# Optimization experiments

Hardware: AMD Instinct MI355X
Metric: run time of the kernel (lower is better)

Reference implementation:

```python
import jax, jax.numpy as jnp
import numpy as np
from jax import lax

B, S, D = 4, 2048, 512          # batch, doc seq len, input_size
Y = 8922                          # num labels (ICD codes)
V, E = 50000, 100                 # vocab, word embed dim
T, K = 32, 9                      # code-title tokens, conv filter size
PAD = K // 2


def setup_inputs() -> dict:
    key = jax.random.key(0)
    ks = jax.random.split(key, 8)
    x = jax.random.normal(ks[0], (B, S, D), dtype=jnp.float32)
    target = jax.random.randint(ks[1], (B, Y), 0, 2).astype(jnp.float32)
    c2title = jax.random.randint(ks[2], (Y, T), 0, V)
    embed_W = jax.random.normal(ks[3], (V, E), dtype=jnp.float32) * 0.1
    conv_w = jax.random.normal(ks[4], (D, E, K), dtype=jnp.float32) * 0.05  # [out, in, k]
    conv_b = jax.random.normal(ks[5], (D,), dtype=jnp.float32) * 0.05
    final_w = jax.random.normal(ks[6], (Y, D), dtype=jnp.float32) * 0.05
    final_b = jax.random.normal(ks[7], (Y,), dtype=jnp.float32) * 0.05
    return {"x": x, "target": target, "c2title": c2title, "embed_W": embed_W,
            "conv_w": conv_w, "conv_b": conv_b, "final_w": final_w, "final_b": final_b}


def reference(x, target, c2title, embed_W, conv_w, conv_b, final_w, final_b):
    # Code-title encoder: embed -> Conv1d (same padding) -> max-pool over time -> tanh
    ct = embed_W[c2title]                      # [Y, T, E]
    ct = jnp.transpose(ct, (0, 2, 1))          # [Y, E, T]  (NCH)
    U = lax.conv_general_dilated(ct, conv_w, window_strides=(1,),
                                 padding=[(PAD, PAD)],
                                 dimension_numbers=("NCH", "OIH", "NCH"))
    U = U + conv_b[None, :, None]              # [Y, D, T]
    U = jnp.tanh(jnp.max(U, axis=-1))          # [Y, D]  (MaxPool1d(T) + tanh)

    # Label cross-attention over document tokens
    scale = 1.0 / jnp.sqrt(jnp.float32(D))
    scores = jnp.einsum("yd,bsd->bys", U, x) * scale   # [B, Y, S]
    alpha = jax.nn.softmax(scores, axis=-1)             # softmax over seq
    m = jnp.einsum("bys,bsd->byd", alpha, x)            # [B, Y, D]

    # Per-label elementwise dot product + bias
    y = jnp.einsum("byd,yd->by", m, final_w) + final_b  # [B, Y]

    # BCEWithLogitsLoss (mean), numerically stable
    loss = jnp.mean(jnp.maximum(y, 0.0) - y * target + jnp.log1p(jnp.exp(-jnp.abs(y))))
    return (y, loss, alpha, m)
```

## Files before the change

kernel.cpp:

```cpp
#include <hip/hip_runtime.h>
#include <math.h>

#define BQ 4
#define SQ 2048
#define DQ 512
#define YQ 8922
#define TQ 32
#define EQ 100
#define EP 128
#define KQ 9
#define LD 128
#define TP 40
#define YPAD 8960

typedef float f32x4 __attribute__((ext_vector_type(4)));
typedef short s16x8 __attribute__((ext_vector_type(8)));

static __device__ __forceinline__ f32x4 mfma16(s16x8 a, s16x8 b, f32x4 c) {
  return __builtin_amdgcn_mfma_f32_16x16x32_bf16(a, b, c, 0, 0, 0);
}

static __device__ __forceinline__ ushort f2bf(float f) {
  union { float f; unsigned u; } v; v.f = f;
  unsigned r = (v.u + 0x7FFFu + ((v.u >> 16) & 1u)) >> 16;
  return (ushort)r;
}

static __device__ __forceinline__ float bf2f(ushort h) {
  union { unsigned u; float f; } v; v.u = ((unsigned)h) << 16; return v.f;
}

static __device__ __forceinline__ f32x4 ld4u(const float* p) {
  f32x4 v; __builtin_memcpy(&v, p, 16); return v;
}

static __device__ __forceinline__ int swz_chunk(int row, int chunk) {
  return chunk ^ (row & 15);
}
static __device__ __forceinline__ int swz3(int row, int chunk) {
  return chunk ^ (row & 7);
}

__global__ void k_prep_x(const float* __restrict__ x, ushort* __restrict__ xb,
                         ushort* __restrict__ xT) {
  __shared__ ushort sm[32][33];
  int b = blockIdx.z;
  int s0 = blockIdx.x * 32;
  int d0 = blockIdx.y * 32;
  int tx = threadIdx.x, ty = threadIdx.y;
  float v = x[((size_t)b * SQ + s0 + ty) * DQ + d0 + tx];
  ushort h = f2bf(v);
  xb[((size_t)b * SQ + s0 + ty) * DQ + d0 + tx] = h;
  sm[ty][tx] = h;
  __syncthreads();
  xT[((size_t)b * DQ + d0 + ty) * SQ + s0 + tx] = sm[tx][ty];
}

__global__ void k_pack_w(const float* __restrict__ cw, ushort* __restrict__ Wp) {
  int i = blockIdx.x * 256 + threadIdx.x;
  if (i >= KQ * DQ * EP) return;
  int e = i & (EP - 1);
  int d = (i >> 7) & (DQ - 1);
  int kk = i >> 16;
  float v = (e < EQ) ? cw[((size_t)d * EQ + e) * KQ + kk] : 0.f;
  Wp[i] = f2bf(v);
}

__launch_bounds__(256, 2)
__global__ void k_conv(const int* __restrict__ c2t, const float* __restrict__ embed,
                       const ushort* __restrict__ Wp, const float* __restrict__ cb,
                       ushort* __restrict__ U) {
  __shared__ ushort sA[4 * TP * LD];
  __shared__ ushort sB[128 * LD];
  const f32x4 fz4 = {0.f, 0.f, 0.f, 0.f};
  int tid = threadIdx.x;
  int d0 = blockIdx.x * 128;
  int y0 = blockIdx.y * 4;
  int lane = tid & 63, wave = tid >> 6;
  int wm = wave & 1, wn = wave >> 1;
  int lr = lane & 15, lg = lane >> 4;

  #pragma unroll
  for (int it = 0; it < 2; ++it) {
    int u = tid + it * 256;
    if (u < 2 * 4 * TP) {
      int row = u >> 1, half = u & 1;
      int yl = row / TP, tt = row - yl * TP;
      int ts = tt - 4;
      int y = y0 + yl;
      const float* src = 0;
      if (y < YQ && (unsigned)ts < (unsigned)TQ)
        src = embed + (size_t)c2t[y * TQ + ts] * EQ + half * 64;
      #pragma unroll
      for (int j = 0; j < 16; ++j) {
        int col = half * 64 + j * 4;
        f32x4 v = fz4;
        if (src != 0 && col + 4 <= EQ) v = *(const f32x4*)(src + j * 4);
        ushort4 h = make_ushort4(f2bf(v.x), f2bf(v.y), f2bf(v.z), f2bf(v.w));
        int pc = swz_chunk(row, col >> 3);
        *(ushort4*)&sA[row * LD + pc * 8 + (col & 7)] = h;
      }
    }
  }

  s16x8 breg[8];
  {
    const ushort* src = Wp + (size_t)d0 * EP;
    #pragma unroll
    for (int it = 0; it < 8; ++it) {
      int gi = tid + it * 256, r = gi >> 4, g = gi & 15;
      breg[it] = *(const s16x8*)(src + (size_t)r * EP + g * 8);
    }
    #pragma unroll
    for (int it = 0; it < 8; ++it) {
      int gi = tid + it * 256, r = gi >> 4, g = gi & 15;
      *(s16x8*)&sB[r * LD + swz_chunk(r, g) * 8] = breg[it];
    }
  }
  __syncthreads();

  f32x4 acc[4][4];
  #pragma unroll
  for (int i = 0; i < 4; ++i)
    #pragma unroll
    for (int j = 0; j < 4; ++j) acc[i][j] = fz4;

  for (int kk = 0; kk < KQ; ++kk) {
    if (kk + 1 < KQ) {
      const ushort* src = Wp + ((size_t)(kk + 1) * DQ + d0) * EP;
      #pragma unroll
      for (int it = 0; it < 8; ++it) {
        int gi = tid + it * 256, r = gi >> 4, g = gi & 15;
        breg[it] = *(const s16x8*)(src + (size_t)r * EP + g * 8);
      }
    }
    #pragma unroll
    for (int ee = 0; ee < 4; ++ee) {
      s16x8 af[4], bfr[4];
      #pragma unroll
      for (int i = 0; i < 4; ++i) {
        int rowm = wm * 64 + i * 16 + lr;
        int yl = rowm >> 5;
        int row = yl * TP + (rowm & 31) + kk;
        af[i] = *(const s16x8*)&sA[row * LD + swz_chunk(row, ee * 4 + lg) * 8];
      }
      #pragma unroll
      for (int i = 0; i < 4; ++i) {
        int row = wn * 64 + i * 16 + lr;
        bfr[i] = *(const s16x8*)&sB[row * LD + swz_chunk(row, ee * 4 + lg) * 8];
      }
      #pragma unroll
      for (int i = 0; i < 4; ++i)
        #pragma unroll
        for (int j = 0; j < 4; ++j)
          acc[i][j] = mfma16(af[i], bfr[j], acc[i][j]);
    }
    __syncthreads();
    if (kk + 1 < KQ) {
      #pragma unroll
      for (int it = 0; it < 8; ++it) {
        int gi = tid + it * 256, r = gi >> 4, g = gi & 15;
        *(s16x8*)&sB[r * LD + swz_chunk(r, g) * 8] = breg[it];
      }
      __syncthreads();
    }
  }

  const float scl = 0.04419417382415922f;
  #pragma unroll
  for (int L2 = 0; L2 < 2; ++L2) {
    int y = y0 + wm * 2 + L2;
    #pragma unroll
    for (int j = 0; j < 4; ++j) {
      float mx = -3.0e38f;
      #pragma unroll
      for (int ii = 0; ii < 2; ++ii)
        #pragma unroll
        for (int q = 0; q < 4; ++q)
          mx = fmaxf(mx, acc[L2 * 2 + ii][j][q]);
      mx = fmaxf(mx, __shfl_xor(mx, 16));
      mx = fmaxf(mx, __shfl_xor(mx, 32));
      if (lane < 16 && y < YQ) {
        int col = d0 + wn * 64 + j * 16 + lane;
        U[(size_t)y * DQ + col] = f2bf(tanhf(mx + cb[col]) * scl);
      }
    }
  }
}

__launch_bounds__(256, 2)
__global__ void k_scores(const ushort* __restrict__ U, const ushort* __restrict__ xb,
                         float* __restrict__ sc, float* __restrict__ part) {
  __shared__ ushort sA[128 * LD];
  __shared__ ushort sB[128 * LD];
  const f32x4 fz4 = {0.f, 0.f, 0.f, 0.f};
  int tid = threadIdx.x;
  int s0 = blockIdx.x * 128;
  int y0 = blockIdx.y * 128;
  int b = blockIdx.z;
  const ushort* Ap = U + (size_t)y0 * DQ;
  const ushort* Bp = xb + ((size_t)b * SQ + s0) * DQ;
  f32x4 acc[4][4];
  #pragma unroll
  for (int i = 0; i < 4; ++i)
    #pragma unroll
    for (int j = 0; j < 4; ++j) acc[i][j] = fz4;
  int lane = tid & 63, wave = tid >> 6;
  int wm = wave & 1, wn = wave >> 1;
  int lr = lane & 15, lg = lane >> 4;

  for (int kc = 0; kc < DQ; kc += 128) {
    __syncthreads();
    #pragma unroll
    for (int it = 0; it < 8; ++it) {
      int gi = tid + it * 256;
      int r = gi >> 4, g = gi & 15;
      int pofs = r * LD + swz_chunk(r, g) * 8;
      *(s16x8*)&sA[pofs] = *(const s16x8*)(Ap + (size_t)r * DQ + kc + g * 8);
      *(s16x8*)&sB[pofs] = *(const s16x8*)(Bp + (size_t)r * DQ + kc + g * 8);
    }
    __syncthreads();
    #pragma unroll
    for (int ks = 0; ks < 4; ++ks) {
      s16x8 af[4], bfr[4];
      #pragma unroll
      for (int i = 0; i < 4; ++i) {
        int row = wm * 64 + i * 16 + lr;
        af[i] = *(const s16x8*)&sA[row * LD + swz_chunk(row, ks * 4 + lg) * 8];
      }
      #pragma unroll
      for (int i = 0; i < 4; ++i) {
        int row = wn * 64 + i * 16 + lr;
        bfr[i] = *(const s16x8*)&sB[row * LD + swz_chunk(row, ks * 4 + lg) * 8];
      }
      #pragma unroll
      for (int i = 0; i < 4; ++i)
        #pragma unroll
        for (int j = 0; j < 4; ++j)
          acc[i][j] = mfma16(af[i], bfr[j], acc[i][j]);
    }
  }
  float* out = sc + (size_t)b * YQ * SQ;
  int rb = wm * 64 + lg * 4;
  int cb_ = wn * 64 + lr;
  #pragma unroll
  for (int i = 0; i < 4; ++i)
    #pragma unroll
    for (int j = 0; j < 4; ++j) {
      int col = s0 + cb_ + j * 16;
      #pragma unroll
      for (int q = 0; q < 4; ++q) {
        int r = y0 + rb + i * 16 + q;
        if (r < YQ) out[(size_t)r * SQ + col] = acc[i][j][q];
      }
    }

  int hb = blockIdx.x * 2 + wn;
  #pragma unroll
  for (int i = 0; i < 4; ++i)
    #pragma unroll
    for (int q = 0; q < 4; ++q) {
      float mx = fmaxf(fmaxf(acc[i][0][q], acc[i][1][q]),
                       fmaxf(acc[i][2][q], acc[i][3][q]));
      #pragma unroll
      for (int o = 1; o < 16; o <<= 1) mx = fmaxf(mx, __shfl_xor(mx, o));
      float se = 0.f;
      #pragma unroll
      for (int j = 0; j < 4; ++j) se += __expf(acc[i][j][q] - mx);
      #pragma unroll
      for (int o = 1; o < 16; o <<= 1) se += __shfl_xor(se, o);
      int r = y0 + rb + i * 16 + q;
      if (lr == 0 && r < YQ) {
        float* pp = part + ((size_t)(b * YQ + r) * 32 + hb) * 2;
        pp[0] = mx;
        pp[1] = se;
      }
    }
}

__global__ void k_smfix(const float* __restrict__ part, float* __restrict__ rs) {
  int t = blockIdx.x * 256 + threadIdx.x;
  if (t >= BQ * YQ) return;
  const float* pp = part + (size_t)t * 64;
  float M = -3.0e38f;
  #pragma unroll
  for (int h = 0; h < 32; ++h) M = fmaxf(M, pp[h * 2]);
  float Z = 0.f;
  #pragma unroll
  for (int h = 0; h < 32; ++h) Z += __expf(pp[h * 2] - M) * pp[h * 2 + 1];
  rs[t * 2] = M;
  rs[t * 2 + 1] = 1.0f / Z;
}

__global__ void k_alpha(float* __restrict__ a, const float* __restrict__ rs,
                        ushort* __restrict__ abf) {
  int r = blockIdx.x;
  float M = rs[r * 2], iZ = rs[r * 2 + 1];
  float* p = a + (size_t)r * SQ;
  int tid = threadIdx.x;
  if (abf) {
    ushort* q = abf + (size_t)r * SQ;
    #pragma unroll
    for (int i = 0; i < 8; ++i) {
      int e = tid + i * 256;
      q[e] = f2bf(__expf(p[e] - M) * iZ);
    }
  } else {
    #pragma unroll
    for (int i = 0; i < 8; ++i) {
      int e = tid + i * 256;
      p[e] = __expf(p[e] - M) * iZ;
    }
  }
}

__launch_bounds__(512, 4)
__global__ void k_pv2(const ushort* __restrict__ abf, const ushort* __restrict__ xT,
                      float* __restrict__ mo, float* __restrict__ aout) {
  __shared__ ushort sA[128 * 64];
  __shared__ ushort sB[256 * 64];
  const f32x4 fz4 = {0.f, 0.f, 0.f, 0.f};
  const s16x8 sz8 = {0, 0, 0, 0, 0, 0, 0, 0};
  int tid = threadIdx.x;
  int d0 = blockIdx.x * 256;
  int y0 = blockIdx.y * 128;
  int b = blockIdx.z;
  int lane = tid & 63, wave = tid >> 6;
  int wm = wave >> 1;
  int wn = wave & 1;
  int lr = lane & 15, lg = lane >> 4;
  bool wr_alpha = (blockIdx.x == 0);

  const ushort* Ap = abf + ((size_t)b * YQ + y0) * SQ;
  const ushort* Bp = xT + ((size_t)b * DQ + d0) * SQ;

  f32x4 acc[2][8];
  #pragma unroll
  for (int i = 0; i < 2; ++i)
    #pragma unroll
    for (int j = 0; j < 8; ++j) acc[i][j] = fz4;

  for (int kc = 0; kc < SQ; kc += 64) {
    #pragma unroll
    for (int p = 0; p < 2; ++p) {
      int u = tid + p * 512;
      int r = u >> 3, c = u & 7;
      int y = y0 + r;
      s16x8 v = sz8;
      if (y < YQ) {
        size_t base = (size_t)r * SQ + kc + c * 8;
        v = *(const s16x8*)(Ap + base);
        if (wr_alpha) {
          float* ao = aout + ((size_t)b * YQ + y) * SQ + kc + c * 8;
          f32x4 w0, w1;
          #pragma unroll
          for (int k2 = 0; k2 < 4; ++k2) w0[k2] = bf2f((ushort)v[k2]);
          #pragma unroll
          for (int k2 = 0; k2 < 4; ++k2) w1[k2] = bf2f((ushort)v[4 + k2]);
          *(f32x4*)ao = w0;
          *(f32x4*)(ao + 4) = w1;
        }
      }
      *(s16x8*)&sA[r * 64 + swz3(r, c) * 8] = v;
    }
    #pragma unroll
    for (int p = 0; p < 4; ++p) {
      int u = tid + p * 512;
      int r = u >> 3, c = u & 7;
      *(s16x8*)&sB[r * 64 + swz3(r, c) * 8] =
          *(const s16x8*)(Bp + (size_t)r * SQ + kc + c * 8);
    }
    __syncthreads();
    #pragma unroll
    for (int ks = 0; ks < 2; ++ks) {
      s16x8 af[2];
      #pragma unroll
      for (int i = 0; i < 2; ++i) {
        int row = wm * 32 + i * 16 + lr;
        af[i] = *(const s16x8*)&sA[row * 64 + swz3(row, ks * 4 + lg) * 8];
      }
      #pragma unroll
      for (int j = 0; j < 8; ++j) {
        int row = wn * 128 + j * 16 + lr;
        s16x8 bf = *(const s16x8*)&sB[row * 64 + swz3(row, ks * 4 + lg) * 8];
        acc[0][j] = mfma16(af[0], bf, acc[0][j]);
        acc[1][j] = mfma16(af[1], bf, acc[1][j]);
      }
    }
    __syncthreads();
  }

  float* out = mo + (size_t)b * YQ * DQ;
  #pragma unroll
  for (int i = 0; i < 2; ++i)
    #pragma unroll
    for (int q = 0; q < 4; ++q) {
      int r = y0 + wm * 32 + i * 16 + lg * 4 + q;
      if (r >= YQ) continue;
      #pragma unroll
      for (int j = 0; j < 8; ++j) {
        int col = d0 + wn * 128 + j * 16 + lr;
        out[(size_t)r * DQ + col] = acc[i][j][q];
      }
    }
}

__launch_bounds__(256, 2)
__global__ void k_pv(const float* __restrict__ alpha, const ushort* __restrict__ xT,
                     float* __restrict__ mo) {
  __shared__ ushort sA[128 * LD];
  __shared__ ushort sB[128 * LD];
  const f32x4 fz4 = {0.f, 0.f, 0.f, 0.f};
  int tid = threadIdx.x;
  int d0 = blockIdx.x * 128;
  int y0 = blockIdx.y * 128;
  int b = blockIdx.z;
  const float* Ap = alpha + ((size_t)b * YQ + y0) * SQ;
  const ushort* Bp = xT + ((size_t)b * DQ + d0) * SQ;
  f32x4 acc[4][4];
  #pragma unroll
  for (int i = 0; i < 4; ++i)
    #pragma unroll
    for (int j = 0; j < 4; ++j) acc[i][j] = fz4;
  int lane = tid & 63, wave = tid >> 6;
  int wm = wave & 1, wn = wave >> 1;
  int lr = lane & 15, lg = lane >> 4;

  for (int kc = 0; kc < SQ; kc += 128) {
    __syncthreads();
    #pragma unroll
    for (int it = 0; it < 8; ++it) {
      int gi = tid + it * 256;
      int r = gi >> 4, g = gi & 15;
      int y = y0 + r;
      int pofs = r * LD + swz_chunk(r, g) * 8;
      ushort4 h0 = make_ushort4(0, 0, 0, 0), h1 = make_ushort4(0, 0, 0, 0);
      if (y < YQ) {
        f32x4 v0 = ld4u(Ap + (size_t)r * SQ + kc + g * 8);
        f32x4 v1 = ld4u(Ap + (size_t)r * SQ + kc + g * 8 + 4);
        h0 = make_ushort4(f2bf(v0.x), f2bf(v0.y), f2bf(v0.z), f2bf(v0.w));
        h1 = make_ushort4(f2bf(v1.x), f2bf(v1.y), f2bf(v1.z), f2bf(v1.w));
      }
      *(ushort4*)&sA[pofs] = h0;
      *(ushort4*)&sA[pofs + 4] = h1;
      *(s16x8*)&sB[pofs] = *(const s16x8*)(Bp + (size_t)r * SQ + kc + g * 8);
    }
    __syncthreads();
    #pragma unroll
    for (int ks = 0; ks < 4; ++ks) {
      s16x8 af[4], bfr[4];
      #pragma unroll
      for (int i = 0; i < 4; ++i) {
        int row = wm * 64 + i * 16 + lr;
        af[i] = *(const s16x8*)&sA[row * LD + swz_chunk(row, ks * 4 + lg) * 8];
      }
      #pragma unroll
      for (int i = 0; i < 4; ++i) {
        int row = wn * 64 + i * 16 + lr;
        bfr[i] = *(const s16x8*)&sB[row * LD + swz_chunk(row, ks * 4 + lg) * 8];
      }
      #pragma unroll
      for (int i = 0; i < 4; ++i)
        #pragma unroll
        for (int j = 0; j < 4; ++j)
          acc[i][j] = mfma16(af[i], bfr[j], acc[i][j]);
    }
  }
  float* out = mo + (size_t)b * YQ * DQ;
  int rb = wm * 64 + lg * 4;
  int cb_ = wn * 64 + lr;
  #pragma unroll
  for (int i = 0; i < 4; ++i)
    #pragma unroll
    for (int j = 0; j < 4; ++j) {
      int col = d0 + cb_ + j * 16;
      #pragma unroll
      for (int q = 0; q < 4; ++q) {
        int r = y0 + rb + i * 16 + q;
        if (r < YQ) out[(size_t)r * DQ + col] = acc[i][j][q];
      }
    }
}

__global__ void k_final(const float* __restrict__ m_in, const float* __restrict__ fw,
                        const float* __restrict__ fb, const float* __restrict__ tgt,
                        float* __restrict__ yo, float* __restrict__ part) {
  int y = blockIdx.x;
  int lane = threadIdx.x & 63;
  int b = threadIdx.x >> 6;
  const float* mp = m_in + ((size_t)b * YQ + y) * DQ;
  const float* wp = fw + (size_t)y * DQ;
  float s = 0.f;
  #pragma unroll
  for (int i = 0; i < 8; ++i) {
    int e = lane + i * 64;
    s += mp[e] * wp[e];
  }
  #pragma unroll
  for (int o = 32; o > 0; o >>= 1) s += __shfl_xor(s, o);
  __shared__ float pl[4];
  if (lane == 0) {
    float yv = s + fb[y];
    yo[(size_t)b * YQ + y] = yv;
    float t = tgt[(size_t)b * YQ + y];
    pl[b] = fmaxf(yv, 0.f) - yv * t + log1pf(__expf(-fabsf(yv)));
  }
  __syncthreads();
  if (threadIdx.x == 0)
    part[y] = (pl[0] + pl[1]) + (pl[2] + pl[3]);
}

__global__ void k_loss_fin(const float* __restrict__ part, float* __restrict__ out) {
  int tid = threadIdx.x;
  float s = 0.f;
  for (int i = tid; i < YQ; i += 256) s += part[i];
  #pragma unroll
  for (int o = 32; o > 0; o >>= 1) s += __shfl_xor(s, o);
  __shared__ float red[4];
  int lane = tid & 63, wave = tid >> 6;
  if (lane == 0) red[wave] = s;
  __syncthreads();
  if (tid == 0)
    out[0] = ((red[0] + red[1]) + (red[2] + red[3])) * (1.0f / (float)(BQ * YQ));
}

extern "C" void kernel_launch(void* const* d_in, const int* in_sizes, int n_in,
                              void* d_out, int out_size, void* d_ws, size_t ws_size,
                              hipStream_t stream) {
  const float* x      = (const float*)d_in[0];
  const float* target = (const float*)d_in[1];
  const int*   c2t    = (const int*)d_in[2];
  const float* embed  = (const float*)d_in[3];
  const float* cw     = (const float*)d_in[4];
  const float* cb     = (const float*)d_in[5];
  const float* fw     = (const float*)d_in[6];
  const float* fb     = (const float*)d_in[7];

  char* ws = (char*)d_ws;
  ushort* xb   = (ushort*)(ws);
  ushort* xT   = (ushort*)(ws + 8388608);
  ushort* Wp   = (ushort*)(ws + 16777216);
  ushort* U    = (ushort*)(ws + 17956864);
  float* lpart = (float*)(ws + 27131904);
  float* part  = (float*)(ws + 27167744);
  float* rst   = (float*)(ws + 36303872);
  const size_t ABF_OFF = 36589568;
  const size_t NEED_ABF = ABF_OFF + (size_t)BQ * YQ * SQ * 2;
  bool use_abf = (ws_size >= NEED_ABF);
  ushort* abf = use_abf ? (ushort*)(ws + ABF_OFF) : (ushort*)0;

  float* out       = (float*)d_out;
  float* out_y     = out;
  float* out_loss  = out + (size_t)BQ * YQ;
  float* out_alpha = out + (size_t)BQ * YQ + 1;
  float* out_m     = out_alpha + (size_t)BQ * YQ * SQ;

  hipMemsetAsync(U, 0, (size_t)YPAD * DQ * 2, stream);

  k_prep_x<<<dim3(SQ / 32, DQ / 32, BQ), dim3(32, 32), 0, stream>>>(x, xb, xT);
  k_pack_w<<<dim3((KQ * DQ * EP + 255) / 256), 256, 0, stream>>>(cw, Wp);
  k_conv<<<dim3(4, (YQ + 3) / 4), 256, 0, stream>>>(c2t, embed, Wp, cb, U);
  k_scores<<<dim3(SQ / 128, (YQ + 127) / 128, BQ), 256, 0, stream>>>(U, xb, out_alpha, part);
  k_smfix<<<dim3((BQ * YQ + 255) / 256), 256, 0, stream>>>(part, rst);
  k_alpha<<<dim3(BQ * YQ), 256, 0, stream>>>(out_alpha, rst, abf);
  if (use_abf)
    k_pv2<<<dim3(DQ / 256, (YQ + 127) / 128, BQ), 512, 0, stream>>>(abf, xT, out_m, out_alpha);
  else
    k_pv<<<dim3(DQ / 128, (YQ + 127) / 128, BQ), 256, 0, stream>>>(out_alpha, xT, out_m);
  k_final<<<dim3(YQ), 256, 0, stream>>>(out_m, fw, fb, target, out_y, lpart);
  k_loss_fin<<<1, 256, 0, stream>>>(lpart, out_loss);
}
```

Before: 997.8 us.

## Enlarge conv tile to 8 labels, double-buffer weights, split alpha writes across blocks

```diff
diff --git a/kernel.cpp b/kernel.cpp
--- a/kernel.cpp
+++ b/kernel.cpp
@@ -10,7 +10,6 @@
 #define EP 128
 #define KQ 9
 #define LD 128
-#define TP 40
 #define YPAD 8960
 
 typedef float f32x4 __attribute__((ext_vector_type(4)));
@@ -66,55 +65,52 @@
   Wp[i] = f2bf(v);
 }
 
-__launch_bounds__(256, 2)
+__launch_bounds__(512, 2)
 __global__ void k_conv(const int* __restrict__ c2t, const float* __restrict__ embed,
                        const ushort* __restrict__ Wp, const float* __restrict__ cb,
                        ushort* __restrict__ U) {
-  __shared__ ushort sA[4 * TP * LD];
-  __shared__ ushort sB[128 * LD];
+  __shared__ ushort sA[8 * TQ * LD];
+  __shared__ ushort sB[2][128 * LD];
   const f32x4 fz4 = {0.f, 0.f, 0.f, 0.f};
+  const s16x8 sz8 = {0, 0, 0, 0, 0, 0, 0, 0};
   int tid = threadIdx.x;
   int d0 = blockIdx.x * 128;
-  int y0 = blockIdx.y * 4;
+  int y0 = blockIdx.y * 8;
   int lane = tid & 63, wave = tid >> 6;
-  int wm = wave & 1, wn = wave >> 1;
+  int wm = wave >> 1;
+  int wn = wave & 1;
   int lr = lane & 15, lg = lane >> 4;
 
-  #pragma unroll
-  for (int it = 0; it < 2; ++it) {
-    int u = tid + it * 256;
-    if (u < 2 * 4 * TP) {
-      int row = u >> 1, half = u & 1;
-      int yl = row / TP, tt = row - yl * TP;
-      int ts = tt - 4;
-      int y = y0 + yl;
-      const float* src = 0;
-      if (y < YQ && (unsigned)ts < (unsigned)TQ)
-        src = embed + (size_t)c2t[y * TQ + ts] * EQ + half * 64;
-      #pragma unroll
-      for (int j = 0; j < 16; ++j) {
-        int col = half * 64 + j * 4;
-        f32x4 v = fz4;
-        if (src != 0 && col + 4 <= EQ) v = *(const f32x4*)(src + j * 4);
-        ushort4 h = make_ushort4(f2bf(v.x), f2bf(v.y), f2bf(v.z), f2bf(v.w));
-        int pc = swz_chunk(row, col >> 3);
-        *(ushort4*)&sA[row * LD + pc * 8 + (col & 7)] = h;
-      }
-    }
-  }
-
-  s16x8 breg[8];
+  {
+    int row = tid >> 1;
+    int half = tid & 1;
+    int yl = row >> 5, t = row & 31;
+    int y = y0 + yl;
+    const float* src = 0;
+    if (y < YQ) src = embed + (size_t)c2t[y * TQ + t] * EQ + half * 64;
+    #pragma unroll
+    for (int j = 0; j < 16; ++j) {
+      int col = half * 64 + j * 4;
+      f32x4 v = fz4;
+      if (src != 0 && col + 4 <= EQ) v = *(const f32x4*)(src + j * 4);
+      ushort4 h = make_ushort4(f2bf(v.x), f2bf(v.y), f2bf(v.z), f2bf(v.w));
+      int pc = swz_chunk(row, col >> 3);
+      *(ushort4*)&sA[row * LD + pc * 8 + (col & 7)] = h;
+    }
+  }
+
+  s16x8 breg[4];
   {
     const ushort* src = Wp + (size_t)d0 * EP;
     #pragma unroll
-    for (int it = 0; it < 8; ++it) {
-      int gi = tid + it * 256, r = gi >> 4, g = gi & 15;
-      breg[it] = *(const s16x8*)(src + (size_t)r * EP + g * 8);
-    }
-    #pragma unroll
-    for (int it = 0; it < 8; ++it) {
-      int gi = tid + it * 256, r = gi >> 4, g = gi & 15;
-      *(s16x8*)&sB[r * LD + swz_chunk(r, g) * 8] = breg[it];
+    for (int p = 0; p < 4; ++p) {
+      int gi = tid + p * 512, r = gi >> 4, g = gi & 15;
+      breg[p] = *(const s16x8*)(src + (size_t)r * EP + g * 8);
+    }
+    #pragma unroll
+    for (int p = 0; p < 4; ++p) {
+      int gi = tid + p * 512, r = gi >> 4, g = gi & 15;
+      *(s16x8*)&sB[0][r * LD + swz_chunk(r, g) * 8] = breg[p];
     }
   }
   __syncthreads();
@@ -129,11 +125,12 @@
     if (kk + 1 < KQ) {
       const ushort* src = Wp + ((size_t)(kk + 1) * DQ + d0) * EP;
       #pragma unroll
-      for (int it = 0; it < 8; ++it) {
-        int gi = tid + it * 256, r = gi >> 4, g = gi & 15;
-        breg[it] = *(const s16x8*)(src + (size_t)r * EP + g * 8);
-      }
-    }
+      for (int p = 0; p < 4; ++p) {
+        int gi = tid + p * 512, r = gi >> 4, g = gi & 15;
+        breg[p] = *(const s16x8*)(src + (size_t)r * EP + g * 8);
+      }
+    }
+    const ushort* sBc = &sB[kk & 1][0];
     #pragma unroll
     for (int ee = 0; ee < 4; ++ee) {
       s16x8 af[4], bfr[4];
@@ -141,13 +138,18 @@
       for (int i = 0; i < 4; ++i) {
         int rowm = wm * 64 + i * 16 + lr;
         int yl = rowm >> 5;
-        int row = yl * TP + (rowm & 31) + kk;
-        af[i] = *(const s16x8*)&sA[row * LD + swz_chunk(row, ee * 4 + lg) * 8];
+        int ts = (rowm & 31) + kk - 4;
+        s16x8 a = sz8;
+        if ((unsigned)ts < (unsigned)TQ) {
+          int row = yl * TQ + ts;
+          a = *(const s16x8*)&sA[row * LD + swz_chunk(row, ee * 4 + lg) * 8];
+        }
+        af[i] = a;
       }
       #pragma unroll
       for (int i = 0; i < 4; ++i) {
         int row = wn * 64 + i * 16 + lr;
-        bfr[i] = *(const s16x8*)&sB[row * LD + swz_chunk(row, ee * 4 + lg) * 8];
+        bfr[i] = *(const s16x8*)&sBc[row * LD + swz_chunk(row, ee * 4 + lg) * 8];
       }
       #pragma unroll
       for (int i = 0; i < 4; ++i)
@@ -155,12 +157,12 @@
         for (int j = 0; j < 4; ++j)
           acc[i][j] = mfma16(af[i], bfr[j], acc[i][j]);
     }
-    __syncthreads();
     if (kk + 1 < KQ) {
-      #pragma unroll
-      for (int it = 0; it < 8; ++it) {
-        int gi = tid + it * 256, r = gi >> 4, g = gi & 15;
-        *(s16x8*)&sB[r * LD + swz_chunk(r, g) * 8] = breg[it];
+      ushort* sBn = &sB[(kk & 1) ^ 1][0];
+      #pragma unroll
+      for (int p = 0; p < 4; ++p) {
+        int gi = tid + p * 512, r = gi >> 4, g = gi & 15;
+        *(s16x8*)&sBn[r * LD + swz_chunk(r, g) * 8] = breg[p];
       }
       __syncthreads();
     }
@@ -329,7 +331,6 @@
   int wm = wave >> 1;
   int wn = wave & 1;
   int lr = lane & 15, lg = lane >> 4;
-  bool wr_alpha = (blockIdx.x == 0);
 
   const ushort* Ap = abf + ((size_t)b * YQ + y0) * SQ;
   const ushort* Bp = xT + ((size_t)b * DQ + d0) * SQ;
@@ -341,6 +342,7 @@
     for (int j = 0; j < 8; ++j) acc[i][j] = fz4;
 
   for (int kc = 0; kc < SQ; kc += 64) {
+    bool wr_alpha = ((kc >> 10) == (int)blockIdx.x);
     #pragma unroll
     for (int p = 0; p < 2; ++p) {
       int u = tid + p * 512;
@@ -559,7 +561,7 @@
 
   k_prep_x<<<dim3(SQ / 32, DQ / 32, BQ), dim3(32, 32), 0, stream>>>(x, xb, xT);
   k_pack_w<<<dim3((KQ * DQ * EP + 255) / 256), 256, 0, stream>>>(cw, Wp);
-  k_conv<<<dim3(4, (YQ + 3) / 4), 256, 0, stream>>>(c2t, embed, Wp, cb, U);
+  k_conv<<<dim3(4, (YQ + 7) / 8), 512, 0, stream>>>(c2t, embed, Wp, cb, U);
   k_scores<<<dim3(SQ / 128, (YQ + 127) / 128, BQ), 256, 0, stream>>>(U, xb, out_alpha, part);
   k_smfix<<<dim3((BQ * YQ + 255) / 256), 256, 0, stream>>>(part, rst);
   k_alpha<<<dim3(BQ * YQ), 256, 0, stream>>>(out_alpha, rst, abf);
```

After: 989.6 us. About the same (-0.8%).
